# Performance work log

Measured on AMD Instinct MI355X. Metric: run time of the kernel, lower is better.

The kernel has to match this reference:

```python
import jax, jax.numpy as jnp
import numpy as np

H = 256          # hidden_size
S = 4            # feature size (2D -> 4)
T_OUT = 16       # args.output // args.skip
HT_LIM = 100.0   # hardtanh limit
B = 16384
OBS = 16


def lstm_cell(x, h, c, Wih, Whh, bih, bhh):
    # PyTorch gate order: i, f, g, o
    g = x @ Wih.T + h @ Whh.T + bih + bhh  # [B, 4H]
    i, f, gg, o = jnp.split(g, 4, axis=-1)
    c = jax.nn.sigmoid(f) * c + jax.nn.sigmoid(i) * jnp.tanh(gg)
    h = jax.nn.sigmoid(o) * jnp.tanh(c)
    return h, c


def encode(seq, Wih, Whh, bih, bhh):
    # seq: [B, T, S]; single-layer LSTM, return final (h, c)
    h0 = jnp.zeros((seq.shape[0], H), seq.dtype)
    def step(carry, x):
        h, c = carry
        return lstm_cell(x, h, c, Wih, Whh, bih, bhh), None
    (h, c), _ = jax.lax.scan(step, (h0, h0), jnp.swapaxes(seq, 0, 1))
    return h, c


def setup_inputs() -> dict:
    key = jax.random.key(0)
    ks = jax.random.split(key, 32)
    sc = 0.05
    def W(k, shape):
        return (jax.random.normal(k, shape, jnp.float32) * sc)
    inp = {
        'speed': jax.random.normal(ks[0], (B, OBS, S), jnp.float32),
        'pos': jax.random.normal(ks[1], (B, OBS, S), jnp.float32),
        # speed encoder LSTM
        'sp_Wih': W(ks[2], (4 * H, S)), 'sp_Whh': W(ks[3], (4 * H, H)),
        'sp_bih': W(ks[4], (4 * H,)), 'sp_bhh': W(ks[5], (4 * H,)),
        # pos encoder LSTM
        'po_Wih': W(ks[6], (4 * H, S)), 'po_Whh': W(ks[7], (4 * H, H)),
        'po_bih': W(ks[8], (4 * H,)), 'po_bhh': W(ks[9], (4 * H,)),
        # speed decoder LSTMCell
        'dsp_Wih': W(ks[10], (4 * H, S)), 'dsp_Whh': W(ks[11], (4 * H, H)),
        'dsp_bih': W(ks[12], (4 * H,)), 'dsp_bhh': W(ks[13], (4 * H,)),
        # crossing decoder LSTMCell
        'dcr_Wih': W(ks[14], (4 * H, S)), 'dcr_Whh': W(ks[15], (4 * H, H)),
        'dcr_bih': W(ks[16], (4 * H,)), 'dcr_bhh': W(ks[17], (4 * H,)),
        # heads
        'fc_speed_W': W(ks[18], (S, H)), 'fc_speed_b': W(ks[19], (S,)),
        'fc_cross_W': W(ks[20], (2, H)), 'fc_cross_b': W(ks[21], (2,)),
        'emb_W': W(ks[22], (S, H)), 'emb_b': W(ks[23], (S,)),
    }
    return inp


def reference(speed, pos,
              sp_Wih, sp_Whh, sp_bih, sp_bhh,
              po_Wih, po_Whh, po_bih, po_bhh,
              dsp_Wih, dsp_Whh, dsp_bih, dsp_bhh,
              dcr_Wih, dcr_Whh, dcr_bih, dcr_bhh,
              fc_speed_W, fc_speed_b, fc_cross_W, fc_cross_b,
              emb_W, emb_b):
    hsp, csp = encode(speed, sp_Wih, sp_Whh, sp_bih, sp_bhh)
    hpo, cpo = encode(pos, po_Wih, po_Whh, po_bih, po_bhh)
    h0 = hpo + hsp
    c0 = cpo + csp

    # ---- speed decoder: feed back hardtanh(fc_speed(h)) (detached) ----
    def sp_step(carry, _):
        h, c, x = carry
        h, c = lstm_cell(x, h, c, dsp_Wih, dsp_Whh, dsp_bih, dsp_bhh)
        out = jnp.clip(h @ fc_speed_W.T + fc_speed_b, -HT_LIM, HT_LIM)
        return (h, c, jax.lax.stop_gradient(out)), out
    _, sp_outs = jax.lax.scan(sp_step, (h0, c0, speed[:, -1, :]), None, length=T_OUT)
    speed_outputs = jnp.swapaxes(sp_outs, 0, 1)  # [B, T_OUT, S]

    # ---- crossing decoder: feed back relu(pos_embedding(h)) (detached) ----
    def cr_step(carry, _):
        h, c, x = carry
        h, c = lstm_cell(x, h, c, dcr_Wih, dcr_Whh, dcr_bih, dcr_bhh)
        logits = jax.nn.relu(h @ fc_cross_W.T + fc_cross_b)  # [B, 2]
        out = jax.nn.softmax(logits, axis=1)
        x_next = jax.lax.stop_gradient(jax.nn.relu(h @ emb_W.T + emb_b))
        return (h, c, x_next), out
    _, cr_outs = jax.lax.scan(cr_step, (h0, c0, pos[:, -1, :]), None, length=T_OUT)
    crossing_outputs = jnp.swapaxes(cr_outs, 0, 1)  # [B, T_OUT, 2]

    return (speed_outputs, crossing_outputs)
```

## Files before the change

### kernel.cpp

```cpp
#include <hip/hip_runtime.h>

typedef unsigned short ushort_t;
typedef __bf16 bf16x8 __attribute__((ext_vector_type(8)));
typedef float f32x4 __attribute__((ext_vector_type(4)));

#define PACK_W_ELEMS (8*9*8*512)
#define HEAD_ELEMS   (9*512)
#define PACK_TOTAL   (4*PACK_W_ELEMS + 2*HEAD_ELEMS)
#define FLAG_OFS     PACK_TOTAL

__device__ __forceinline__ float bf2f(ushort_t u){ return __uint_as_float(((unsigned)u)<<16); }
__device__ __forceinline__ ushort_t f2bf(float f){
  __bf16 h = (__bf16)f;
  return *(ushort_t*)&h;
}
__device__ __forceinline__ float rcp_(float x){ return __builtin_amdgcn_rcpf(x); }
__device__ __forceinline__ float sigmf_(float x){ return rcp_(1.0f + __expf(-x)); }
__device__ __forceinline__ float tanhf_(float x){ return 1.0f - 2.0f*rcp_(1.0f + __expf(2.0f*x)); }

__device__ __forceinline__ int sniff_f32(const ushort_t* w){
  int f32 = 0;
  #pragma unroll
  for (int i = 0; i < 32; ++i){
    float f = bf2f(w[2*i]);
    if (!(f > -8.f && f < 8.f)) f32 = 1;
  }
  return f32;
}
__device__ __forceinline__ float ldin(const ushort_t* p, int i, int f32){
  return f32 ? ((const float*)p)[i] : bf2f(p[i]);
}
__device__ __forceinline__ ushort_t ldw(const ushort_t* p, int i, int f32){
  return f32 ? f2bf(((const float*)p)[i]) : p[i];
}

struct PackArgs {
  const ushort_t* wih[4]; const ushort_t* whh[4];
  const ushort_t* bih[4]; const ushort_t* bhh[4];
  const ushort_t* fcsp_w; const ushort_t* fcsp_b;
  const ushort_t* fccr_w; const ushort_t* fccr_b;
  const ushort_t* emb_w;  const ushort_t* emb_b;
  ushort_t* ws;
};

__global__ void pack_kernel(PackArgs a){
  const int f32 = sniff_f32(a.whh[0]);
  int idx = blockIdx.x*256 + threadIdx.x;
  if (blockIdx.x == 0 && threadIdx.x == 0) *(int*)(a.ws + FLAG_OFS) = f32;
  const int total_w = 4*PACK_W_ELEMS;
  if (idx < total_w){
    int l = idx / PACK_W_ELEMS;
    int r = idx % PACK_W_ELEMS;
    int j = r & 7;
    int lane = (r>>3) & 63;
    int tile = r >> 9;
    int gu = tile & 7;
    int kt = (tile >> 3) % 9;
    int wv = tile / 72;
    int g = gu >> 1, u = gu & 1;
    int n = (g*16 + wv*2 + u)*16 + (lane & 15);
    int k = kt*32 + ((lane>>4)<<3) + j;
    ushort_t v = 0;
    if (k < 256)       v = ldw(a.whh[l], n*256 + k, f32);
    else if (k < 260)  v = ldw(a.wih[l], n*4 + (k-256), f32);
    else if (k == 260) v = f2bf(ldin(a.bih[l], n, f32) + ldin(a.bhh[l], n, f32));
    a.ws[l*PACK_W_ELEMS + r] = v;
    return;
  }
  idx -= total_w;
  if (idx < 2*HEAD_ELEMS){
    int which = idx / HEAD_ELEMS;
    int r = idx % HEAD_ELEMS;
    int j = r & 7; int lane = (r>>3)&63; int kt = r>>9;
    int n = lane & 15; int k = kt*32 + ((lane>>4)<<3) + j;
    ushort_t v = 0;
    if (which == 0){
      if (n < 4){
        if (k < 256)       v = ldw(a.fcsp_w, n*256 + k, f32);
        else if (k == 260) v = f2bf(ldin(a.fcsp_b, n, f32));
      }
    } else {
      if (n < 4){
        if (k < 256)       v = ldw(a.emb_w, n*256 + k, f32);
        else if (k == 260) v = f2bf(ldin(a.emb_b, n, f32));
      } else if (n < 6){
        if (k < 256)       v = ldw(a.fccr_w, (n-4)*256 + k, f32);
        else if (k == 260) v = f2bf(ldin(a.fccr_b, n-4, f32));
      }
    }
    a.ws[total_w + idx] = v;
  }
}

__device__ __forceinline__ void gate_gemm(const ushort_t* __restrict__ Aln,
                                          const ushort_t* __restrict__ bw,
                                          f32x4 (&acc)[4][8], int lane){
  #pragma unroll
  for (int i = 0; i < 4; ++i)
    #pragma unroll
    for (int j = 0; j < 8; ++j) acc[i][j] = (f32x4){0.f,0.f,0.f,0.f};
  bf16x8 p0 = *(const bf16x8*)&bw[0*512];
  bf16x8 p1 = *(const bf16x8*)&bw[1*512];
  bf16x8 p2 = *(const bf16x8*)&bw[2*512];
  bf16x8 p3 = *(const bf16x8*)&bw[3*512];
  const ushort_t* bp = bw;
  #pragma unroll 1
  for (int kt = 0; kt < 9; ++kt){
    bf16x8 q0 = *(const bf16x8*)&bp[4*512];
    bf16x8 q1 = *(const bf16x8*)&bp[5*512];
    bf16x8 q2 = *(const bf16x8*)&bp[6*512];
    bf16x8 q3 = *(const bf16x8*)&bp[7*512];
    bf16x8 a0 = *(const bf16x8*)&Aln[(0*9+kt)*512];
    bf16x8 a1 = *(const bf16x8*)&Aln[(1*9+kt)*512];
    bf16x8 a2 = *(const bf16x8*)&Aln[(2*9+kt)*512];
    bf16x8 a3 = *(const bf16x8*)&Aln[(3*9+kt)*512];
    acc[0][0] = __builtin_amdgcn_mfma_f32_16x16x32_bf16(a0, p0, acc[0][0], 0, 0, 0);
    acc[1][0] = __builtin_amdgcn_mfma_f32_16x16x32_bf16(a1, p0, acc[1][0], 0, 0, 0);
    acc[2][0] = __builtin_amdgcn_mfma_f32_16x16x32_bf16(a2, p0, acc[2][0], 0, 0, 0);
    acc[3][0] = __builtin_amdgcn_mfma_f32_16x16x32_bf16(a3, p0, acc[3][0], 0, 0, 0);
    acc[0][1] = __builtin_amdgcn_mfma_f32_16x16x32_bf16(a0, p1, acc[0][1], 0, 0, 0);
    acc[1][1] = __builtin_amdgcn_mfma_f32_16x16x32_bf16(a1, p1, acc[1][1], 0, 0, 0);
    acc[2][1] = __builtin_amdgcn_mfma_f32_16x16x32_bf16(a2, p1, acc[2][1], 0, 0, 0);
    acc[3][1] = __builtin_amdgcn_mfma_f32_16x16x32_bf16(a3, p1, acc[3][1], 0, 0, 0);
    acc[0][2] = __builtin_amdgcn_mfma_f32_16x16x32_bf16(a0, p2, acc[0][2], 0, 0, 0);
    acc[1][2] = __builtin_amdgcn_mfma_f32_16x16x32_bf16(a1, p2, acc[1][2], 0, 0, 0);
    acc[2][2] = __builtin_amdgcn_mfma_f32_16x16x32_bf16(a2, p2, acc[2][2], 0, 0, 0);
    acc[3][2] = __builtin_amdgcn_mfma_f32_16x16x32_bf16(a3, p2, acc[3][2], 0, 0, 0);
    acc[0][3] = __builtin_amdgcn_mfma_f32_16x16x32_bf16(a0, p3, acc[0][3], 0, 0, 0);
    acc[1][3] = __builtin_amdgcn_mfma_f32_16x16x32_bf16(a1, p3, acc[1][3], 0, 0, 0);
    acc[2][3] = __builtin_amdgcn_mfma_f32_16x16x32_bf16(a2, p3, acc[2][3], 0, 0, 0);
    acc[3][3] = __builtin_amdgcn_mfma_f32_16x16x32_bf16(a3, p3, acc[3][3], 0, 0, 0);
    if (kt < 8){
      p0 = *(const bf16x8*)&bp[4096 + 0*512];
      p1 = *(const bf16x8*)&bp[4096 + 1*512];
      p2 = *(const bf16x8*)&bp[4096 + 2*512];
      p3 = *(const bf16x8*)&bp[4096 + 3*512];
    }
    acc[0][4] = __builtin_amdgcn_mfma_f32_16x16x32_bf16(a0, q0, acc[0][4], 0, 0, 0);
    acc[1][4] = __builtin_amdgcn_mfma_f32_16x16x32_bf16(a1, q0, acc[1][4], 0, 0, 0);
    acc[2][4] = __builtin_amdgcn_mfma_f32_16x16x32_bf16(a2, q0, acc[2][4], 0, 0, 0);
    acc[3][4] = __builtin_amdgcn_mfma_f32_16x16x32_bf16(a3, q0, acc[3][4], 0, 0, 0);
    acc[0][5] = __builtin_amdgcn_mfma_f32_16x16x32_bf16(a0, q1, acc[0][5], 0, 0, 0);
    acc[1][5] = __builtin_amdgcn_mfma_f32_16x16x32_bf16(a1, q1, acc[1][5], 0, 0, 0);
    acc[2][5] = __builtin_amdgcn_mfma_f32_16x16x32_bf16(a2, q1, acc[2][5], 0, 0, 0);
    acc[3][5] = __builtin_amdgcn_mfma_f32_16x16x32_bf16(a3, q1, acc[3][5], 0, 0, 0);
    acc[0][6] = __builtin_amdgcn_mfma_f32_16x16x32_bf16(a0, q2, acc[0][6], 0, 0, 0);
    acc[1][6] = __builtin_amdgcn_mfma_f32_16x16x32_bf16(a1, q2, acc[1][6], 0, 0, 0);
    acc[2][6] = __builtin_amdgcn_mfma_f32_16x16x32_bf16(a2, q2, acc[2][6], 0, 0, 0);
    acc[3][6] = __builtin_amdgcn_mfma_f32_16x16x32_bf16(a3, q2, acc[3][6], 0, 0, 0);
    acc[0][7] = __builtin_amdgcn_mfma_f32_16x16x32_bf16(a0, q3, acc[0][7], 0, 0, 0);
    acc[1][7] = __builtin_amdgcn_mfma_f32_16x16x32_bf16(a1, q3, acc[1][7], 0, 0, 0);
    acc[2][7] = __builtin_amdgcn_mfma_f32_16x16x32_bf16(a2, q3, acc[2][7], 0, 0, 0);
    acc[3][7] = __builtin_amdgcn_mfma_f32_16x16x32_bf16(a3, q3, acc[3][7], 0, 0, 0);
    bp += 4096;
  }
}

__device__ __forceinline__ void gates_wb(f32x4 (&acc)[4][8], float (&cw)[4][2][4],
                                         ushort_t* __restrict__ Ap, int wbBase){
  #pragma unroll
  for (int mt = 0; mt < 4; ++mt)
    #pragma unroll
    for (int u = 0; u < 2; ++u)
      #pragma unroll
      for (int r = 0; r < 4; ++r){
        float cn = sigmf_(acc[mt][2+u][r])*cw[mt][u][r]
                 + sigmf_(acc[mt][u][r])*tanhf_(acc[mt][4+u][r]);
        float hn = sigmf_(acc[mt][6+u][r])*tanhf_(cn);
        cw[mt][u][r] = cn;
        Ap[mt*4608 + u*256 + r*8 + wbBase] = f2bf(hn);
      }
}

__global__ __launch_bounds__(512, 2) void pvlstm_main(
    const ushort_t* __restrict__ ws,
    const ushort_t* __restrict__ speed,
    const ushort_t* __restrict__ pos,
    void* __restrict__ outv)
{
  __shared__ ushort_t ApS[4*9*512];
  __shared__ ushort_t ApP[4*9*512];
  __shared__ ushort_t xsS[64*64];
  __shared__ ushort_t xsP[64*64];
  __shared__ float    ostS[64*64];
  __shared__ float    ostC[64*32];

  const int f32   = *(const int*)(ws + FLAG_OFS);
  const int tid   = threadIdx.x;
  const int lane  = tid & 63;
  const int w     = tid >> 6;
  const int col16 = lane & 15;
  const int quad  = lane >> 4;
  const int brow0 = blockIdx.x * 64;
  const int wbBase = w*512 + (col16>>3)*128 + quad*32 + (col16&7);

  ushort_t* outu = (ushort_t*)outv;
  float*    outf = (float*)outv;

  const ushort_t* headsp = ws + 4*PACK_W_ELEMS;
  const ushort_t* headcr = headsp + HEAD_ELEMS;
  const ushort_t* aS  = ApS + lane*8;
  const ushort_t* aP  = ApP + lane*8;
  const ushort_t* bwS  = ws + 0*PACK_W_ELEMS + (size_t)w*36864 + (size_t)lane*8;
  const ushort_t* bwP  = ws + 1*PACK_W_ELEMS + (size_t)w*36864 + (size_t)lane*8;
  const ushort_t* bwDS = ws + 2*PACK_W_ELEMS + (size_t)w*36864 + (size_t)lane*8;
  const ushort_t* bwDC = ws + 3*PACK_W_ELEMS + (size_t)w*36864 + (size_t)lane*8;

  float cwA[4][2][4], cwB[4][2][4];
  f32x4 acc[4][8];

  for (int i = tid; i < 4096; i += 512){
    int gi = (brow0 + (i>>6))*64 + (i&63);
    xsS[i] = f2bf(ldin(speed, gi, f32));
    xsP[i] = f2bf(ldin(pos,   gi, f32));
  }
  for (int i = tid; i < 4*9*512/2; i += 512){
    ((unsigned*)ApS)[i] = 0u; ((unsigned*)ApP)[i] = 0u;
  }
  #pragma unroll
  for (int mt = 0; mt < 4; ++mt)
    #pragma unroll
    for (int u = 0; u < 2; ++u)
      #pragma unroll
      for (int r = 0; r < 4; ++r){ cwA[mt][u][r] = 0.f; cwB[mt][u][r] = 0.f; }
  __syncthreads();
  if (tid < 64){
    ushort_t* xpS = &ApS[((tid>>4)*9 + 8)*512 + (tid&15)*8];
    ushort_t* xpP = &ApP[((tid>>4)*9 + 8)*512 + (tid&15)*8];
    *(uint2*)xpS = *(const uint2*)&xsS[tid*64];
    xpS[4] = (ushort_t)0x3f80;
    xpP[4] = (ushort_t)0x3f80;
  }
  __syncthreads();

  for (int t = 0; t < 16; ++t){
    if (t > 0) gates_wb(acc, cwB, ApP, wbBase);
    if (tid < 64)
      *(uint2*)&ApP[((tid>>4)*9 + 8)*512 + (tid&15)*8] = *(const uint2*)&xsP[tid*64 + t*4];
    gate_gemm(aS, bwS, acc, lane);
    __syncthreads();
    gates_wb(acc, cwA, ApS, wbBase);
    if (t < 15 && tid < 64)
      *(uint2*)&ApS[((tid>>4)*9 + 8)*512 + (tid&15)*8] = *(const uint2*)&xsS[tid*64 + t*4 + 4];
    gate_gemm(aP, bwP, acc, lane);
    __syncthreads();
  }
  #pragma unroll
  for (int mt = 0; mt < 4; ++mt)
    #pragma unroll
    for (int u = 0; u < 2; ++u)
      #pragma unroll
      for (int r = 0; r < 4; ++r){
        float cn = sigmf_(acc[mt][2+u][r])*cwB[mt][u][r]
                 + sigmf_(acc[mt][u][r])*tanhf_(acc[mt][4+u][r]);
        float hn = sigmf_(acc[mt][6+u][r])*tanhf_(cn);
        float c0 = cwA[mt][u][r] + cn;
        cwA[mt][u][r] = c0; cwB[mt][u][r] = c0;
        const int ad = mt*4608 + u*256 + r*8 + wbBase;
        ushort_t h0 = f2bf(bf2f(ApS[ad]) + hn);
        ApS[ad] = h0; ApP[ad] = h0;
      }
  if (tid < 64){
    *(uint2*)&ApS[((tid>>4)*9 + 8)*512 + (tid&15)*8] = *(const uint2*)&xsS[tid*64 + 60];
    *(uint2*)&ApP[((tid>>4)*9 + 8)*512 + (tid&15)*8] = *(const uint2*)&xsP[tid*64 + 60];
  }
  __syncthreads();

  for (int t = 0; t < 16; ++t){
    if (t > 0 && w >= 4){
      const int mt = w - 4;
      f32x4 hacc = (f32x4){0.f,0.f,0.f,0.f};
      #pragma unroll
      for (int kt = 0; kt < 9; ++kt){
        bf16x8 a  = *(const bf16x8*)&aP[(mt*9+kt)*512];
        bf16x8 bv = *(const bf16x8*)&headcr[((size_t)kt*64 + lane)*8];
        hacc = __builtin_amdgcn_mfma_f32_16x16x32_bf16(a, bv, hacc, 0, 0, 0);
      }
      const int s = col16;
      #pragma unroll
      for (int r = 0; r < 4; ++r){
        float v = fmaxf(hacc[r], 0.f);
        const float o = __shfl_xor(v, 1, 64);
        const int m = mt*16 + quad*4 + r;
        if (s < 4){
          ApP[(mt*9+8)*512 + (m&15)*8 + s] = f2bf(v);
        } else if (s < 6){
          const float mx = fmaxf(v, o);
          const float e0 = __expf(v-mx), e1 = __expf(o-mx);
          ostC[m*32 + (t-1)*2 + (s-4)] = e0*rcp_(e0+e1);
        }
      }
    }
    gate_gemm(aS, bwDS, acc, lane);
    __syncthreads();
    gates_wb(acc, cwA, ApS, wbBase);
    gate_gemm(aP, bwDC, acc, lane);
    __syncthreads();
    gates_wb(acc, cwB, ApP, wbBase);
    if (w < 4){
      const int mt = w;
      f32x4 hacc = (f32x4){0.f,0.f,0.f,0.f};
      #pragma unroll
      for (int kt = 0; kt < 9; ++kt){
        bf16x8 a  = *(const bf16x8*)&aS[(mt*9+kt)*512];
        bf16x8 bv = *(const bf16x8*)&headsp[((size_t)kt*64 + lane)*8];
        hacc = __builtin_amdgcn_mfma_f32_16x16x32_bf16(a, bv, hacc, 0, 0, 0);
      }
      const int s = col16;
      if (s < 4){
        #pragma unroll
        for (int r = 0; r < 4; ++r){
          float v = fminf(fmaxf(hacc[r], -100.f), 100.f);
          const int m = mt*16 + quad*4 + r;
          ostS[m*64 + t*4 + s] = v;
          ApS[(mt*9+8)*512 + (m&15)*8 + s] = f2bf(v);
        }
      }
    }
    __syncthreads();
  }
  if (w >= 4){
    const int mt = w - 4;
    f32x4 hacc = (f32x4){0.f,0.f,0.f,0.f};
    #pragma unroll
    for (int kt = 0; kt < 9; ++kt){
      bf16x8 a  = *(const bf16x8*)&aP[(mt*9+kt)*512];
      bf16x8 bv = *(const bf16x8*)&headcr[((size_t)kt*64 + lane)*8];
      hacc = __builtin_amdgcn_mfma_f32_16x16x32_bf16(a, bv, hacc, 0, 0, 0);
    }
    const int s = col16;
    if (s >= 4 && s < 6){
      #pragma unroll
      for (int r = 0; r < 4; ++r){
        float v = fmaxf(hacc[r], 0.f);
        const float o = __shfl_xor(v, 1, 64);
        const int m = mt*16 + quad*4 + r;
        const float mx = fmaxf(v, o);
        const float e0 = __expf(v-mx), e1 = __expf(o-mx);
        ostC[m*32 + 15*2 + (s-4)] = e0*rcp_(e0+e1);
      }
    }
  }
  __syncthreads();

  for (int i = tid; i < 4096; i += 512){
    const int oi = (brow0 + (i>>6))*64 + (i&63);
    const float v = ostS[i];
    if (f32) outf[oi] = v; else outu[oi] = f2bf(v);
  }
  for (int i = tid; i < 2048; i += 512){
    const int oi = 1048576 + (brow0 + (i>>5))*32 + (i&31);
    const float v = ostC[i];
    if (f32) outf[oi] = v; else outu[oi] = f2bf(v);
  }
}

extern "C" void kernel_launch(void* const* d_in, const int* in_sizes, int n_in,
                              void* d_out, int out_size, void* d_ws, size_t ws_size,
                              hipStream_t stream) {
  PackArgs pa;
  pa.wih[0]=(const ushort_t*)d_in[2];  pa.whh[0]=(const ushort_t*)d_in[3];
  pa.bih[0]=(const ushort_t*)d_in[4];  pa.bhh[0]=(const ushort_t*)d_in[5];
  pa.wih[1]=(const ushort_t*)d_in[6];  pa.whh[1]=(const ushort_t*)d_in[7];
  pa.bih[1]=(const ushort_t*)d_in[8];  pa.bhh[1]=(const ushort_t*)d_in[9];
  pa.wih[2]=(const ushort_t*)d_in[10]; pa.whh[2]=(const ushort_t*)d_in[11];
  pa.bih[2]=(const ushort_t*)d_in[12]; pa.bhh[2]=(const ushort_t*)d_in[13];
  pa.wih[3]=(const ushort_t*)d_in[14]; pa.whh[3]=(const ushort_t*)d_in[15];
  pa.bih[3]=(const ushort_t*)d_in[16]; pa.bhh[3]=(const ushort_t*)d_in[17];
  pa.fcsp_w=(const ushort_t*)d_in[18]; pa.fcsp_b=(const ushort_t*)d_in[19];
  pa.fccr_w=(const ushort_t*)d_in[20]; pa.fccr_b=(const ushort_t*)d_in[21];
  pa.emb_w =(const ushort_t*)d_in[22]; pa.emb_b =(const ushort_t*)d_in[23];
  pa.ws = (ushort_t*)d_ws;

  hipLaunchKernelGGL(pack_kernel, dim3((PACK_TOTAL + 255)/256), dim3(256), 0, stream, pa);
  hipLaunchKernelGGL(pvlstm_main, dim3(256), dim3(512), 0, stream,
      (const ushort_t*)d_ws,
      (const ushort_t*)d_in[0], (const ushort_t*)d_in[1],
      d_out);
}
```

Before: 851.8 us.

## Interleave LSTM gate activations with MFMA gate GEMM across passes

Replaces the separate gate GEMM plus writeback with a fused step. The i/f/g gate columns are computed first, then the o-gate columns, with the cell update interleaved into the o-gate MFMA loop. The previous stream's hidden-state writeback is interleaved into the i/f/g loop, so transcendental math overlaps with matrix-core work instead of running serially between barriers. It also switches input loads and output stores to nontemporal hints. In exchange the loops are fully unrolled, which raises register pressure, and the cross-stream state handoff (cwX/cwY swaps) becomes more intricate.

Result: slower. 3.040 ms (+256.9%).

```diff
diff --git a/kernel.cpp b/kernel.cpp
--- a/kernel.cpp
+++ b/kernel.cpp
@@ -29,6 +29,10 @@
 }
 __device__ __forceinline__ float ldin(const ushort_t* p, int i, int f32){
   return f32 ? ((const float*)p)[i] : bf2f(p[i]);
+}
+__device__ __forceinline__ float ldin_nt(const ushort_t* p, int i, int f32){
+  return f32 ? __builtin_nontemporal_load((const float*)p + i)
+             : bf2f(__builtin_nontemporal_load(p + i));
 }
 __device__ __forceinline__ ushort_t ldw(const ushort_t* p, int i, int f32){
   return f32 ? f2bf(((const float*)p)[i]) : p[i];
@@ -92,84 +96,104 @@
   }
 }
 
-__device__ __forceinline__ void gate_gemm(const ushort_t* __restrict__ Aln,
-                                          const ushort_t* __restrict__ bw,
-                                          f32x4 (&acc)[4][8], int lane){
+template<int HN>
+__device__ __forceinline__ void fused_step(
+    const ushort_t* __restrict__ Aln,
+    const ushort_t* __restrict__ bw,
+    f32x4 (&acc)[4][8],
+    float (&cwX)[4][2][4],
+    float (&cwY)[4][2][4],
+    ushort_t* __restrict__ ApY,
+    int wbBase)
+{
   #pragma unroll
-  for (int i = 0; i < 4; ++i)
-    #pragma unroll
-    for (int j = 0; j < 8; ++j) acc[i][j] = (f32x4){0.f,0.f,0.f,0.f};
-  bf16x8 p0 = *(const bf16x8*)&bw[0*512];
-  bf16x8 p1 = *(const bf16x8*)&bw[1*512];
-  bf16x8 p2 = *(const bf16x8*)&bw[2*512];
-  bf16x8 p3 = *(const bf16x8*)&bw[3*512];
-  const ushort_t* bp = bw;
-  #pragma unroll 1
   for (int kt = 0; kt < 9; ++kt){
-    bf16x8 q0 = *(const bf16x8*)&bp[4*512];
-    bf16x8 q1 = *(const bf16x8*)&bp[5*512];
-    bf16x8 q2 = *(const bf16x8*)&bp[6*512];
-    bf16x8 q3 = *(const bf16x8*)&bp[7*512];
+    const ushort_t* bp = bw + kt*4096;
+    bf16x8 b0 = *(const bf16x8*)&bp[0*512];
+    bf16x8 b1 = *(const bf16x8*)&bp[1*512];
+    bf16x8 b2 = *(const bf16x8*)&bp[2*512];
+    bf16x8 b3 = *(const bf16x8*)&bp[3*512];
+    bf16x8 b4 = *(const bf16x8*)&bp[4*512];
+    bf16x8 b5 = *(const bf16x8*)&bp[5*512];
     bf16x8 a0 = *(const bf16x8*)&Aln[(0*9+kt)*512];
     bf16x8 a1 = *(const bf16x8*)&Aln[(1*9+kt)*512];
     bf16x8 a2 = *(const bf16x8*)&Aln[(2*9+kt)*512];
     bf16x8 a3 = *(const bf16x8*)&Aln[(3*9+kt)*512];
-    acc[0][0] = __builtin_amdgcn_mfma_f32_16x16x32_bf16(a0, p0, acc[0][0], 0, 0, 0);
-    acc[1][0] = __builtin_amdgcn_mfma_f32_16x16x32_bf16(a1, p0, acc[1][0], 0, 0, 0);
-    acc[2][0] = __builtin_amdgcn_mfma_f32_16x16x32_bf16(a2, p0, acc[2][0], 0, 0, 0);
-    acc[3][0] = __builtin_amdgcn_mfma_f32_16x16x32_bf16(a3, p0, acc[3][0], 0, 0, 0);
-    acc[0][1] = __builtin_amdgcn_mfma_f32_16x16x32_bf16(a0, p1, acc[0][1], 0, 0, 0);
-    acc[1][1] = __builtin_amdgcn_mfma_f32_16x16x32_bf16(a1, p1, acc[1][1], 0, 0, 0);
-    acc[2][1] = __builtin_amdgcn_mfma_f32_16x16x32_bf16(a2, p1, acc[2][1], 0, 0, 0);
-    acc[3][1] = __builtin_amdgcn_mfma_f32_16x16x32_bf16(a3, p1, acc[3][1], 0, 0, 0);
-    acc[0][2] = __builtin_amdgcn_mfma_f32_16x16x32_bf16(a0, p2, acc[0][2], 0, 0, 0);
-    acc[1][2] = __builtin_amdgcn_mfma_f32_16x16x32_bf16(a1, p2, acc[1][2], 0, 0, 0);
-    acc[2][2] = __builtin_amdgcn_mfma_f32_16x16x32_bf16(a2, p2, acc[2][2], 0, 0, 0);
-    acc[3][2] = __builtin_amdgcn_mfma_f32_16x16x32_bf16(a3, p2, acc[3][2], 0, 0, 0);
-    acc[0][3] = __builtin_amdgcn_mfma_f32_16x16x32_bf16(a0, p3, acc[0][3], 0, 0, 0);
-    acc[1][3] = __builtin_amdgcn_mfma_f32_16x16x32_bf16(a1, p3, acc[1][3], 0, 0, 0);
-    acc[2][3] = __builtin_amdgcn_mfma_f32_16x16x32_bf16(a2, p3, acc[2][3], 0, 0, 0);
-    acc[3][3] = __builtin_amdgcn_mfma_f32_16x16x32_bf16(a3, p3, acc[3][3], 0, 0, 0);
+    if (kt == 0){
+      #pragma unroll
+      for (int i = 0; i < 4; ++i)
+        #pragma unroll
+        for (int j = 0; j < 6; ++j) acc[i][j] = (f32x4){0.f,0.f,0.f,0.f};
+    }
+    acc[0][0] = __builtin_amdgcn_mfma_f32_16x16x32_bf16(a0, b0, acc[0][0], 0, 0, 0);
+    acc[1][0] = __builtin_amdgcn_mfma_f32_16x16x32_bf16(a1, b0, acc[1][0], 0, 0, 0);
+    acc[2][0] = __builtin_amdgcn_mfma_f32_16x16x32_bf16(a2, b0, acc[2][0], 0, 0, 0);
+    acc[3][0] = __builtin_amdgcn_mfma_f32_16x16x32_bf16(a3, b0, acc[3][0], 0, 0, 0);
+    acc[0][1] = __builtin_amdgcn_mfma_f32_16x16x32_bf16(a0, b1, acc[0][1], 0, 0, 0);
+    acc[1][1] = __builtin_amdgcn_mfma_f32_16x16x32_bf16(a1, b1, acc[1][1], 0, 0, 0);
+    acc[2][1] = __builtin_amdgcn_mfma_f32_16x16x32_bf16(a2, b1, acc[2][1], 0, 0, 0);
+    acc[3][1] = __builtin_amdgcn_mfma_f32_16x16x32_bf16(a3, b1, acc[3][1], 0, 0, 0);
+    acc[0][2] = __builtin_amdgcn_mfma_f32_16x16x32_bf16(a0, b2, acc[0][2], 0, 0, 0);
+    acc[1][2] = __builtin_amdgcn_mfma_f32_16x16x32_bf16(a1, b2, acc[1][2], 0, 0, 0);
+    acc[2][2] = __builtin_amdgcn_mfma_f32_16x16x32_bf16(a2, b2, acc[2][2], 0, 0, 0);
+    acc[3][2] = __builtin_amdgcn_mfma_f32_16x16x32_bf16(a3, b2, acc[3][2], 0, 0, 0);
+    acc[0][3] = __builtin_amdgcn_mfma_f32_16x16x32_bf16(a0, b3, acc[0][3], 0, 0, 0);
+    acc[1][3] = __builtin_amdgcn_mfma_f32_16x16x32_bf16(a1, b3, acc[1][3], 0, 0, 0);
+    acc[2][3] = __builtin_amdgcn_mfma_f32_16x16x32_bf16(a2, b3, acc[2][3], 0, 0, 0);
+    acc[3][3] = __builtin_amdgcn_mfma_f32_16x16x32_bf16(a3, b3, acc[3][3], 0, 0, 0);
+    acc[0][4] = __builtin_amdgcn_mfma_f32_16x16x32_bf16(a0, b4, acc[0][4], 0, 0, 0);
+    acc[1][4] = __builtin_amdgcn_mfma_f32_16x16x32_bf16(a1, b4, acc[1][4], 0, 0, 0);
+    acc[2][4] = __builtin_amdgcn_mfma_f32_16x16x32_bf16(a2, b4, acc[2][4], 0, 0, 0);
+    acc[3][4] = __builtin_amdgcn_mfma_f32_16x16x32_bf16(a3, b4, acc[3][4], 0, 0, 0);
+    acc[0][5] = __builtin_amdgcn_mfma_f32_16x16x32_bf16(a0, b5, acc[0][5], 0, 0, 0);
+    acc[1][5] = __builtin_amdgcn_mfma_f32_16x16x32_bf16(a1, b5, acc[1][5], 0, 0, 0);
+    acc[2][5] = __builtin_amdgcn_mfma_f32_16x16x32_bf16(a2, b5, acc[2][5], 0, 0, 0);
+    acc[3][5] = __builtin_amdgcn_mfma_f32_16x16x32_bf16(a3, b5, acc[3][5], 0, 0, 0);
+    if (HN && kt >= 1){
+      #pragma unroll
+      for (int ee = 0; ee < 4; ++ee){
+        const int e  = (kt-1)*4 + ee;
+        const int mt = e >> 3, u = (e >> 2) & 1, r = e & 3;
+        const float hn = sigmf_(acc[mt][6+u][r]) * tanhf_(cwY[mt][u][r]);
+        ApY[mt*4608 + u*256 + r*8 + wbBase] = f2bf(hn);
+      }
+    }
+  }
+  #pragma unroll
+  for (int kt = 0; kt < 9; ++kt){
+    const ushort_t* bp = bw + kt*4096;
+    bf16x8 b6 = *(const bf16x8*)&bp[6*512];
+    bf16x8 b7 = *(const bf16x8*)&bp[7*512];
+    bf16x8 a0 = *(const bf16x8*)&Aln[(0*9+kt)*512];
+    bf16x8 a1 = *(const bf16x8*)&Aln[(1*9+kt)*512];
+    bf16x8 a2 = *(const bf16x8*)&Aln[(2*9+kt)*512];
+    bf16x8 a3 = *(const bf16x8*)&Aln[(3*9+kt)*512];
+    if (kt == 0){
+      #pragma unroll
+      for (int i = 0; i < 4; ++i){
+        acc[i][6] = (f32x4){0.f,0.f,0.f,0.f};
+        acc[i][7] = (f32x4){0.f,0.f,0.f,0.f};
+      }
+    }
+    acc[0][6] = __builtin_amdgcn_mfma_f32_16x16x32_bf16(a0, b6, acc[0][6], 0, 0, 0);
+    acc[1][6] = __builtin_amdgcn_mfma_f32_16x16x32_bf16(a1, b6, acc[1][6], 0, 0, 0);
+    acc[2][6] = __builtin_amdgcn_mfma_f32_16x16x32_bf16(a2, b6, acc[2][6], 0, 0, 0);
+    acc[3][6] = __builtin_amdgcn_mfma_f32_16x16x32_bf16(a3, b6, acc[3][6], 0, 0, 0);
+    acc[0][7] = __builtin_amdgcn_mfma_f32_16x16x32_bf16(a0, b7, acc[0][7], 0, 0, 0);
+    acc[1][7] = __builtin_amdgcn_mfma_f32_16x16x32_bf16(a1, b7, acc[1][7], 0, 0, 0);
+    acc[2][7] = __builtin_amdgcn_mfma_f32_16x16x32_bf16(a2, b7, acc[2][7], 0, 0, 0);
+    acc[3][7] = __builtin_amdgcn_mfma_f32_16x16x32_bf16(a3, b7, acc[3][7], 0, 0, 0);
     if (kt < 8){
-      p0 = *(const bf16x8*)&bp[4096 + 0*512];
-      p1 = *(const bf16x8*)&bp[4096 + 1*512];
-      p2 = *(const bf16x8*)&bp[4096 + 2*512];
-      p3 = *(const bf16x8*)&bp[4096 + 3*512];
-    }
-    acc[0][4] = __builtin_amdgcn_mfma_f32_16x16x32_bf16(a0, q0, acc[0][4], 0, 0, 0);
-    acc[1][4] = __builtin_amdgcn_mfma_f32_16x16x32_bf16(a1, q0, acc[1][4], 0, 0, 0);
-    acc[2][4] = __builtin_amdgcn_mfma_f32_16x16x32_bf16(a2, q0, acc[2][4], 0, 0, 0);
-    acc[3][4] = __builtin_amdgcn_mfma_f32_16x16x32_bf16(a3, q0, acc[3][4], 0, 0, 0);
-    acc[0][5] = __builtin_amdgcn_mfma_f32_16x16x32_bf16(a0, q1, acc[0][5], 0, 0, 0);
-    acc[1][5] = __builtin_amdgcn_mfma_f32_16x16x32_bf16(a1, q1, acc[1][5], 0, 0, 0);
-    acc[2][5] = __builtin_amdgcn_mfma_f32_16x16x32_bf16(a2, q1, acc[2][5], 0, 0, 0);
-    acc[3][5] = __builtin_amdgcn_mfma_f32_16x16x32_bf16(a3, q1, acc[3][5], 0, 0, 0);
-    acc[0][6] = __builtin_amdgcn_mfma_f32_16x16x32_bf16(a0, q2, acc[0][6], 0, 0, 0);
-    acc[1][6] = __builtin_amdgcn_mfma_f32_16x16x32_bf16(a1, q2, acc[1][6], 0, 0, 0);
-    acc[2][6] = __builtin_amdgcn_mfma_f32_16x16x32_bf16(a2, q2, acc[2][6], 0, 0, 0);
-    acc[3][6] = __builtin_amdgcn_mfma_f32_16x16x32_bf16(a3, q2, acc[3][6], 0, 0, 0);
-    acc[0][7] = __builtin_amdgcn_mfma_f32_16x16x32_bf16(a0, q3, acc[0][7], 0, 0, 0);
-    acc[1][7] = __builtin_amdgcn_mfma_f32_16x16x32_bf16(a1, q3, acc[1][7], 0, 0, 0);
-    acc[2][7] = __builtin_amdgcn_mfma_f32_16x16x32_bf16(a2, q3, acc[2][7], 0, 0, 0);
-    acc[3][7] = __builtin_amdgcn_mfma_f32_16x16x32_bf16(a3, q3, acc[3][7], 0, 0, 0);
-    bp += 4096;
-  }
-}
-
-__device__ __forceinline__ void gates_wb(f32x4 (&acc)[4][8], float (&cw)[4][2][4],
-                                         ushort_t* __restrict__ Ap, int wbBase){
-  #pragma unroll
-  for (int mt = 0; mt < 4; ++mt)
-    #pragma unroll
-    for (int u = 0; u < 2; ++u)
-      #pragma unroll
-      for (int r = 0; r < 4; ++r){
-        float cn = sigmf_(acc[mt][2+u][r])*cw[mt][u][r]
-                 + sigmf_(acc[mt][u][r])*tanhf_(acc[mt][4+u][r]);
-        float hn = sigmf_(acc[mt][6+u][r])*tanhf_(cn);
-        cw[mt][u][r] = cn;
-        Ap[mt*4608 + u*256 + r*8 + wbBase] = f2bf(hn);
-      }
+      #pragma unroll
+      for (int ee = 0; ee < 4; ++ee){
+        const int e  = kt*4 + ee;
+        const int mt = e >> 3, u = (e >> 2) & 1, r = e & 3;
+        const float cn = sigmf_(acc[mt][2+u][r]) * cwX[mt][u][r]
+                       + sigmf_(acc[mt][u][r])   * tanhf_(acc[mt][4+u][r]);
+        cwX[mt][u][r] = cn;
+      }
+    }
+  }
 }
 
 __global__ __launch_bounds__(512, 2) void pvlstm_main(
@@ -211,8 +235,8 @@
 
   for (int i = tid; i < 4096; i += 512){
     int gi = (brow0 + (i>>6))*64 + (i&63);
-    xsS[i] = f2bf(ldin(speed, gi, f32));
-    xsP[i] = f2bf(ldin(pos,   gi, f32));
+    xsS[i] = f2bf(ldin_nt(speed, gi, f32));
+    xsP[i] = f2bf(ldin_nt(pos,   gi, f32));
   }
   for (int i = tid; i < 4*9*512/2; i += 512){
     ((unsigned*)ApS)[i] = 0u; ((unsigned*)ApP)[i] = 0u;
@@ -234,15 +258,14 @@
   __syncthreads();
 
   for (int t = 0; t < 16; ++t){
-    if (t > 0) gates_wb(acc, cwB, ApP, wbBase);
     if (tid < 64)
       *(uint2*)&ApP[((tid>>4)*9 + 8)*512 + (tid&15)*8] = *(const uint2*)&xsP[tid*64 + t*4];
-    gate_gemm(aS, bwS, acc, lane);
+    if (t > 0) fused_step<1>(aS, bwS, acc, cwA, cwB, ApP, wbBase);
+    else       fused_step<0>(aS, bwS, acc, cwA, cwB, ApP, wbBase);
     __syncthreads();
-    gates_wb(acc, cwA, ApS, wbBase);
     if (t < 15 && tid < 64)
       *(uint2*)&ApS[((tid>>4)*9 + 8)*512 + (tid&15)*8] = *(const uint2*)&xsS[tid*64 + t*4 + 4];
-    gate_gemm(aP, bwP, acc, lane);
+    fused_step<1>(aP, bwP, acc, cwB, cwA, ApS, wbBase);
     __syncthreads();
   }
   #pragma unroll
@@ -251,10 +274,8 @@
     for (int u = 0; u < 2; ++u)
       #pragma unroll
       for (int r = 0; r < 4; ++r){
-        float cn = sigmf_(acc[mt][2+u][r])*cwB[mt][u][r]
-                 + sigmf_(acc[mt][u][r])*tanhf_(acc[mt][4+u][r]);
-        float hn = sigmf_(acc[mt][6+u][r])*tanhf_(cn);
-        float c0 = cwA[mt][u][r] + cn;
+        float hn = sigmf_(acc[mt][6+u][r]) * tanhf_(cwB[mt][u][r]);
+        float c0 = cwA[mt][u][r] + cwB[mt][u][r];
         cwA[mt][u][r] = c0; cwB[mt][u][r] = c0;
         const int ad = mt*4608 + u*256 + r*8 + wbBase;
         ushort_t h0 = f2bf(bf2f(ApS[ad]) + hn);
@@ -291,12 +312,19 @@
         }
       }
     }
-    gate_gemm(aS, bwDS, acc, lane);
+    fused_step<0>(aS, bwDS, acc, cwA, cwB, ApP, wbBase);
     __syncthreads();
-    gates_wb(acc, cwA, ApS, wbBase);
-    gate_gemm(aP, bwDC, acc, lane);
+    fused_step<1>(aP, bwDC, acc, cwB, cwA, ApS, wbBase);
     __syncthreads();
-    gates_wb(acc, cwB, ApP, wbBase);
+    #pragma unroll
+    for (int mt = 0; mt < 4; ++mt)
+      #pragma unroll
+      for (int u = 0; u < 2; ++u)
+        #pragma unroll
+        for (int r = 0; r < 4; ++r){
+          const float hn = sigmf_(acc[mt][6+u][r]) * tanhf_(cwB[mt][u][r]);
+          ApP[mt*4608 + u*256 + r*8 + wbBase] = f2bf(hn);
+        }
     if (w < 4){
       const int mt = w;
       f32x4 hacc = (f32x4){0.f,0.f,0.f,0.f};
@@ -346,12 +374,14 @@
   for (int i = tid; i < 4096; i += 512){
     const int oi = (brow0 + (i>>6))*64 + (i&63);
     const float v = ostS[i];
-    if (f32) outf[oi] = v; else outu[oi] = f2bf(v);
+    if (f32) __builtin_nontemporal_store(v, outf + oi);
+    else     __builtin_nontemporal_store(f2bf(v), outu + oi);
   }
   for (int i = tid; i < 2048; i += 512){
     const int oi = 1048576 + (brow0 + (i>>5))*32 + (i&31);
     const float v = ostC[i];
-    if (f32) outf[oi] = v; else outu[oi] = f2bf(v);
+    if (f32) __builtin_nontemporal_store(v, outf + oi);
+    else     __builtin_nontemporal_store(f2bf(v), outu + oi);
   }
 }
 
```

## Halve batch rows per block and double grid for higher occupancy

Applied to the files above, without the earlier changes.

Each block now handles 32 batch rows instead of 64. The per-wave accumulator tile shrinks from 4x8 to 2x8 and all LDS buffers are halved. Launch bounds are raised to 4 waves per execution unit and the grid is doubled to 512 blocks, so more waves are resident per CU to hide the latency of weight loads from global memory. The trade-off is that each weight fragment fetched is reused across half as many rows, so total weight traffic through L2 doubles. Input loads and output stores also switch to nontemporal hints.

After: 1.129 ms. 32.5% more time.

```diff
diff --git a/kernel.cpp b/kernel.cpp
--- a/kernel.cpp
+++ b/kernel.cpp
@@ -29,6 +29,10 @@
 }
 __device__ __forceinline__ float ldin(const ushort_t* p, int i, int f32){
   return f32 ? ((const float*)p)[i] : bf2f(p[i]);
+}
+__device__ __forceinline__ float ldin_nt(const ushort_t* p, int i, int f32){
+  return f32 ? __builtin_nontemporal_load((const float*)p + i)
+             : bf2f(__builtin_nontemporal_load(p + i));
 }
 __device__ __forceinline__ ushort_t ldw(const ushort_t* p, int i, int f32){
   return f32 ? f2bf(((const float*)p)[i]) : p[i];
@@ -94,9 +98,9 @@
 
 __device__ __forceinline__ void gate_gemm(const ushort_t* __restrict__ Aln,
                                           const ushort_t* __restrict__ bw,
-                                          f32x4 (&acc)[4][8], int lane){
-  #pragma unroll
-  for (int i = 0; i < 4; ++i)
+                                          f32x4 (&acc)[2][8]){
+  #pragma unroll
+  for (int i = 0; i < 2; ++i)
     #pragma unroll
     for (int j = 0; j < 8; ++j) acc[i][j] = (f32x4){0.f,0.f,0.f,0.f};
   bf16x8 p0 = *(const bf16x8*)&bw[0*512];
@@ -112,24 +116,14 @@
     bf16x8 q3 = *(const bf16x8*)&bp[7*512];
     bf16x8 a0 = *(const bf16x8*)&Aln[(0*9+kt)*512];
     bf16x8 a1 = *(const bf16x8*)&Aln[(1*9+kt)*512];
-    bf16x8 a2 = *(const bf16x8*)&Aln[(2*9+kt)*512];
-    bf16x8 a3 = *(const bf16x8*)&Aln[(3*9+kt)*512];
     acc[0][0] = __builtin_amdgcn_mfma_f32_16x16x32_bf16(a0, p0, acc[0][0], 0, 0, 0);
     acc[1][0] = __builtin_amdgcn_mfma_f32_16x16x32_bf16(a1, p0, acc[1][0], 0, 0, 0);
-    acc[2][0] = __builtin_amdgcn_mfma_f32_16x16x32_bf16(a2, p0, acc[2][0], 0, 0, 0);
-    acc[3][0] = __builtin_amdgcn_mfma_f32_16x16x32_bf16(a3, p0, acc[3][0], 0, 0, 0);
     acc[0][1] = __builtin_amdgcn_mfma_f32_16x16x32_bf16(a0, p1, acc[0][1], 0, 0, 0);
     acc[1][1] = __builtin_amdgcn_mfma_f32_16x16x32_bf16(a1, p1, acc[1][1], 0, 0, 0);
-    acc[2][1] = __builtin_amdgcn_mfma_f32_16x16x32_bf16(a2, p1, acc[2][1], 0, 0, 0);
-    acc[3][1] = __builtin_amdgcn_mfma_f32_16x16x32_bf16(a3, p1, acc[3][1], 0, 0, 0);
     acc[0][2] = __builtin_amdgcn_mfma_f32_16x16x32_bf16(a0, p2, acc[0][2], 0, 0, 0);
     acc[1][2] = __builtin_amdgcn_mfma_f32_16x16x32_bf16(a1, p2, acc[1][2], 0, 0, 0);
-    acc[2][2] = __builtin_amdgcn_mfma_f32_16x16x32_bf16(a2, p2, acc[2][2], 0, 0, 0);
-    acc[3][2] = __builtin_amdgcn_mfma_f32_16x16x32_bf16(a3, p2, acc[3][2], 0, 0, 0);
     acc[0][3] = __builtin_amdgcn_mfma_f32_16x16x32_bf16(a0, p3, acc[0][3], 0, 0, 0);
     acc[1][3] = __builtin_amdgcn_mfma_f32_16x16x32_bf16(a1, p3, acc[1][3], 0, 0, 0);
-    acc[2][3] = __builtin_amdgcn_mfma_f32_16x16x32_bf16(a2, p3, acc[2][3], 0, 0, 0);
-    acc[3][3] = __builtin_amdgcn_mfma_f32_16x16x32_bf16(a3, p3, acc[3][3], 0, 0, 0);
     if (kt < 8){
       p0 = *(const bf16x8*)&bp[4096 + 0*512];
       p1 = *(const bf16x8*)&bp[4096 + 1*512];
@@ -138,28 +132,20 @@
     }
     acc[0][4] = __builtin_amdgcn_mfma_f32_16x16x32_bf16(a0, q0, acc[0][4], 0, 0, 0);
     acc[1][4] = __builtin_amdgcn_mfma_f32_16x16x32_bf16(a1, q0, acc[1][4], 0, 0, 0);
-    acc[2][4] = __builtin_amdgcn_mfma_f32_16x16x32_bf16(a2, q0, acc[2][4], 0, 0, 0);
-    acc[3][4] = __builtin_amdgcn_mfma_f32_16x16x32_bf16(a3, q0, acc[3][4], 0, 0, 0);
     acc[0][5] = __builtin_amdgcn_mfma_f32_16x16x32_bf16(a0, q1, acc[0][5], 0, 0, 0);
     acc[1][5] = __builtin_amdgcn_mfma_f32_16x16x32_bf16(a1, q1, acc[1][5], 0, 0, 0);
-    acc[2][5] = __builtin_amdgcn_mfma_f32_16x16x32_bf16(a2, q1, acc[2][5], 0, 0, 0);
-    acc[3][5] = __builtin_amdgcn_mfma_f32_16x16x32_bf16(a3, q1, acc[3][5], 0, 0, 0);
     acc[0][6] = __builtin_amdgcn_mfma_f32_16x16x32_bf16(a0, q2, acc[0][6], 0, 0, 0);
     acc[1][6] = __builtin_amdgcn_mfma_f32_16x16x32_bf16(a1, q2, acc[1][6], 0, 0, 0);
-    acc[2][6] = __builtin_amdgcn_mfma_f32_16x16x32_bf16(a2, q2, acc[2][6], 0, 0, 0);
-    acc[3][6] = __builtin_amdgcn_mfma_f32_16x16x32_bf16(a3, q2, acc[3][6], 0, 0, 0);
     acc[0][7] = __builtin_amdgcn_mfma_f32_16x16x32_bf16(a0, q3, acc[0][7], 0, 0, 0);
     acc[1][7] = __builtin_amdgcn_mfma_f32_16x16x32_bf16(a1, q3, acc[1][7], 0, 0, 0);
-    acc[2][7] = __builtin_amdgcn_mfma_f32_16x16x32_bf16(a2, q3, acc[2][7], 0, 0, 0);
-    acc[3][7] = __builtin_amdgcn_mfma_f32_16x16x32_bf16(a3, q3, acc[3][7], 0, 0, 0);
     bp += 4096;
   }
 }
 
-__device__ __forceinline__ void gates_wb(f32x4 (&acc)[4][8], float (&cw)[4][2][4],
+__device__ __forceinline__ void gates_wb(f32x4 (&acc)[2][8], float (&cw)[2][2][4],
                                          ushort_t* __restrict__ Ap, int wbBase){
   #pragma unroll
-  for (int mt = 0; mt < 4; ++mt)
+  for (int mt = 0; mt < 2; ++mt)
     #pragma unroll
     for (int u = 0; u < 2; ++u)
       #pragma unroll
@@ -172,18 +158,18 @@
       }
 }
 
-__global__ __launch_bounds__(512, 2) void pvlstm_main(
+__global__ __launch_bounds__(512, 4) void pvlstm_main(
     const ushort_t* __restrict__ ws,
     const ushort_t* __restrict__ speed,
     const ushort_t* __restrict__ pos,
     void* __restrict__ outv)
 {
-  __shared__ ushort_t ApS[4*9*512];
-  __shared__ ushort_t ApP[4*9*512];
-  __shared__ ushort_t xsS[64*64];
-  __shared__ ushort_t xsP[64*64];
-  __shared__ float    ostS[64*64];
-  __shared__ float    ostC[64*32];
+  __shared__ ushort_t ApS[2*9*512];
+  __shared__ ushort_t ApP[2*9*512];
+  __shared__ ushort_t xsS[32*64];
+  __shared__ ushort_t xsP[32*64];
+  __shared__ float    ostS[32*64];
+  __shared__ float    ostC[32*32];
 
   const int f32   = *(const int*)(ws + FLAG_OFS);
   const int tid   = threadIdx.x;
@@ -191,7 +177,7 @@
   const int w     = tid >> 6;
   const int col16 = lane & 15;
   const int quad  = lane >> 4;
-  const int brow0 = blockIdx.x * 64;
+  const int brow0 = blockIdx.x * 32;
   const int wbBase = w*512 + (col16>>3)*128 + quad*32 + (col16&7);
 
   ushort_t* outu = (ushort_t*)outv;
@@ -206,25 +192,25 @@
   const ushort_t* bwDS = ws + 2*PACK_W_ELEMS + (size_t)w*36864 + (size_t)lane*8;
   const ushort_t* bwDC = ws + 3*PACK_W_ELEMS + (size_t)w*36864 + (size_t)lane*8;
 
-  float cwA[4][2][4], cwB[4][2][4];
-  f32x4 acc[4][8];
-
-  for (int i = tid; i < 4096; i += 512){
+  float cwA[2][2][4], cwB[2][2][4];
+  f32x4 acc[2][8];
+
+  for (int i = tid; i < 2048; i += 512){
     int gi = (brow0 + (i>>6))*64 + (i&63);
-    xsS[i] = f2bf(ldin(speed, gi, f32));
-    xsP[i] = f2bf(ldin(pos,   gi, f32));
-  }
-  for (int i = tid; i < 4*9*512/2; i += 512){
+    xsS[i] = f2bf(ldin_nt(speed, gi, f32));
+    xsP[i] = f2bf(ldin_nt(pos,   gi, f32));
+  }
+  for (int i = tid; i < 2*9*512/2; i += 512){
     ((unsigned*)ApS)[i] = 0u; ((unsigned*)ApP)[i] = 0u;
   }
   #pragma unroll
-  for (int mt = 0; mt < 4; ++mt)
+  for (int mt = 0; mt < 2; ++mt)
     #pragma unroll
     for (int u = 0; u < 2; ++u)
       #pragma unroll
       for (int r = 0; r < 4; ++r){ cwA[mt][u][r] = 0.f; cwB[mt][u][r] = 0.f; }
   __syncthreads();
-  if (tid < 64){
+  if (tid < 32){
     ushort_t* xpS = &ApS[((tid>>4)*9 + 8)*512 + (tid&15)*8];
     ushort_t* xpP = &ApP[((tid>>4)*9 + 8)*512 + (tid&15)*8];
     *(uint2*)xpS = *(const uint2*)&xsS[tid*64];
@@ -235,18 +221,18 @@
 
   for (int t = 0; t < 16; ++t){
     if (t > 0) gates_wb(acc, cwB, ApP, wbBase);
-    if (tid < 64)
+    if (tid < 32)
       *(uint2*)&ApP[((tid>>4)*9 + 8)*512 + (tid&15)*8] = *(const uint2*)&xsP[tid*64 + t*4];
-    gate_gemm(aS, bwS, acc, lane);
+    gate_gemm(aS, bwS, acc);
     __syncthreads();
     gates_wb(acc, cwA, ApS, wbBase);
-    if (t < 15 && tid < 64)
+    if (t < 15 && tid < 32)
       *(uint2*)&ApS[((tid>>4)*9 + 8)*512 + (tid&15)*8] = *(const uint2*)&xsS[tid*64 + t*4 + 4];
-    gate_gemm(aP, bwP, acc, lane);
-    __syncthreads();
-  }
-  #pragma unroll
-  for (int mt = 0; mt < 4; ++mt)
+    gate_gemm(aP, bwP, acc);
+    __syncthreads();
+  }
+  #pragma unroll
+  for (int mt = 0; mt < 2; ++mt)
     #pragma unroll
     for (int u = 0; u < 2; ++u)
       #pragma unroll
@@ -260,14 +246,14 @@
         ushort_t h0 = f2bf(bf2f(ApS[ad]) + hn);
         ApS[ad] = h0; ApP[ad] = h0;
       }
-  if (tid < 64){
+  if (tid < 32){
     *(uint2*)&ApS[((tid>>4)*9 + 8)*512 + (tid&15)*8] = *(const uint2*)&xsS[tid*64 + 60];
     *(uint2*)&ApP[((tid>>4)*9 + 8)*512 + (tid&15)*8] = *(const uint2*)&xsP[tid*64 + 60];
   }
   __syncthreads();
 
   for (int t = 0; t < 16; ++t){
-    if (t > 0 && w >= 4){
+    if (t > 0 && w >= 4 && w < 6){
       const int mt = w - 4;
       f32x4 hacc = (f32x4){0.f,0.f,0.f,0.f};
       #pragma unroll
@@ -291,13 +277,13 @@
         }
       }
     }
-    gate_gemm(aS, bwDS, acc, lane);
+    gate_gemm(aS, bwDS, acc);
     __syncthreads();
     gates_wb(acc, cwA, ApS, wbBase);
-    gate_gemm(aP, bwDC, acc, lane);
+    gate_gemm(aP, bwDC, acc);
     __syncthreads();
     gates_wb(acc, cwB, ApP, wbBase);
-    if (w < 4){
+    if (w < 2){
       const int mt = w;
       f32x4 hacc = (f32x4){0.f,0.f,0.f,0.f};
       #pragma unroll
@@ -319,7 +305,7 @@
     }
     __syncthreads();
   }
-  if (w >= 4){
+  if (w >= 4 && w < 6){
     const int mt = w - 4;
     f32x4 hacc = (f32x4){0.f,0.f,0.f,0.f};
     #pragma unroll
@@ -343,15 +329,17 @@
   }
   __syncthreads();
 
-  for (int i = tid; i < 4096; i += 512){
+  for (int i = tid; i < 2048; i += 512){
     const int oi = (brow0 + (i>>6))*64 + (i&63);
     const float v = ostS[i];
-    if (f32) outf[oi] = v; else outu[oi] = f2bf(v);
-  }
-  for (int i = tid; i < 2048; i += 512){
+    if (f32) __builtin_nontemporal_store(v, outf + oi);
+    else     __builtin_nontemporal_store(f2bf(v), outu + oi);
+  }
+  for (int i = tid; i < 1024; i += 512){
     const int oi = 1048576 + (brow0 + (i>>5))*32 + (i&31);
     const float v = ostC[i];
-    if (f32) outf[oi] = v; else outu[oi] = f2bf(v);
+    if (f32) __builtin_nontemporal_store(v, outf + oi);
+    else     __builtin_nontemporal_store(f2bf(v), outu + oi);
   }
 }
 
@@ -373,7 +361,7 @@
   pa.ws = (ushort_t*)d_ws;
 
   hipLaunchKernelGGL(pack_kernel, dim3((PACK_TOTAL + 255)/256), dim3(256), 0, stream, pa);
-  hipLaunchKernelGGL(pvlstm_main, dim3(256), dim3(512), 0, stream,
+  hipLaunchKernelGGL(pvlstm_main, dim3(512), dim3(512), 0, stream,
       (const ushort_t*)d_ws,
       (const ushort_t*)d_in[0], (const ushort_t*)d_in[1],
       d_out);
```
